# Performance work log

Measured on AMD Instinct MI355X. Metric: run time of the kernel, lower is better.

## Reference

```python
import jax, jax.numpy as jnp
import numpy as np


def setup_inputs() -> dict:
    key = jax.random.key(0)
    k1, k2 = jax.random.split(key)
    B, La, Lb, D = 32, 512, 512, 768
    a_bar = jax.random.normal(k1, (B, La, D), dtype=jnp.float32)
    b_bar = jax.random.normal(k2, (B, Lb, D), dtype=jnp.float32)
    return {"a_bar": a_bar, "b_bar": b_bar}


def reference(a_bar, b_bar):
    # e: [B, La, Lb] cross-attention scores
    e = jnp.einsum('bad,bcd->bac', a_bar, b_bar)
    # attend over b positions (softmax dim=2) -> aligned representation of a
    a_tilde = jnp.einsum('bac,bcd->bad', jax.nn.softmax(e, axis=2), b_bar)
    # attend over a positions (softmax dim=1), transpose, bmm with a_bar
    b_tilde = jnp.einsum('bac,bad->bcd', jax.nn.softmax(e, axis=1), a_bar)
    m_a = jnp.concatenate([a_bar, a_tilde, a_bar - a_tilde, a_bar * a_tilde], axis=-1)
    m_b = jnp.concatenate([b_bar, b_tilde, b_bar - b_tilde, b_bar * b_tilde], axis=-1)
    return (m_a, m_b)
```

## Files before the change

kernel.cpp:

```cpp
#include <hip/hip_runtime.h>
#include <hip/hip_bf16.h>
#include <math.h>

#define NB 32
#define LA 512
#define LB 512
#define DD 768

typedef __bf16 bf16x4 __attribute__((ext_vector_type(4)));
typedef __bf16 bf16x8 __attribute__((ext_vector_type(8)));
typedef float f32x4 __attribute__((ext_vector_type(4)));

#define LSTR 40

__device__ __forceinline__ void gload_lds16(const void* g, void* l) {
  __builtin_amdgcn_global_load_lds(
      (const __attribute__((address_space(1))) unsigned int*)g,
      (__attribute__((address_space(3))) unsigned int*)l, 16, 0, 0);
}

__global__ __launch_bounds__(256) void convert_kernel(
    const float* __restrict__ A, const float* __restrict__ B,
    __bf16* __restrict__ Ah, __bf16* __restrict__ Al,
    __bf16* __restrict__ Bh, __bf16* __restrict__ Bl,
    __bf16* __restrict__ AhT, __bf16* __restrict__ BhT) {
  const int zb = blockIdx.z;
  const int b = zb & (NB - 1);
  const bool isB = zb >= NB;
  const float* src = (isB ? B : A) + (size_t)b * 512 * DD;
  __bf16* H = (isB ? Bh : Ah) + (size_t)b * 512 * DD;
  __bf16* L = (isB ? Bl : Al) + (size_t)b * 512 * DD;
  __bf16* T = (isB ? BhT : AhT) + (size_t)b * DD * 512;
  const int d0 = blockIdx.x * 64, i0 = blockIdx.y * 64;
  __shared__ __bf16 Tt[64][72];
  const int t = threadIdx.x;
  const int c4 = t & 15, r = t >> 4;
#pragma unroll
  for (int p = 0; p < 4; ++p) {
    const int i = i0 + r + p * 16;
    const float4 v = *(const float4*)(src + (size_t)i * DD + d0 + c4 * 4);
    float vv[4] = {v.x, v.y, v.z, v.w};
    bf16x4 h, l;
#pragma unroll
    for (int q = 0; q < 4; ++q) {
      h[q] = (__bf16)vv[q];
      l[q] = (__bf16)(vv[q] - (float)h[q]);
    }
    *(bf16x4*)(H + (size_t)i * DD + d0 + c4 * 4) = h;
    *(bf16x4*)(L + (size_t)i * DD + d0 + c4 * 4) = l;
#pragma unroll
    for (int q = 0; q < 4; ++q) Tt[c4 * 4 + q][r + p * 16] = h[q];
  }
  __syncthreads();
  const int cc = t & 7, rr = t >> 3;
#pragma unroll
  for (int p = 0; p < 2; ++p) {
    const int d = d0 + rr + p * 32;
    *(bf16x8*)(T + (size_t)d * 512 + i0 + cc * 8) =
        *(bf16x8*)&Tt[rr + p * 32][cc * 8];
  }
}

__global__ __launch_bounds__(256) void gemm_e_mfma(
    const __bf16* __restrict__ Ah, const __bf16* __restrict__ Al,
    const __bf16* __restrict__ Bh, const __bf16* __restrict__ Bl,
    float* __restrict__ E) {
  __shared__ __bf16 S[2][4][128][32];

  const int id = blockIdx.x;
  const int wg = (id & 7) * 64 + (id >> 3);
  const int b = wg >> 4, tl = wg & 15;
  const int i0 = (tl & 3) * 128, j0 = (tl >> 2) * 128;

  const __bf16* AhB = Ah + (size_t)b * LA * DD;
  const __bf16* AlB = Al + (size_t)b * LA * DD;
  const __bf16* BhB = Bh + (size_t)b * LB * DD;
  const __bf16* BlB = Bl + (size_t)b * LB * DD;
  float* Eb = E + (size_t)b * LA * LB;

  const int t = threadIdx.x;
  const int lane = t & 63, wave = t >> 6;
  const int wm = (wave >> 1) * 64, wn = (wave & 1) * 64;
  const int quad = lane >> 4, l16 = lane & 15;
  const int lrow = lane >> 2, lcol = (lane & 3) * 8;

  auto stage = [&](int buf, int k0) {
#pragma unroll
    for (int n = 0; n < 2; ++n) {
      const int c = n * 4 + wave;
      const int row = c * 16 + lrow;
      const size_t gA = (size_t)(i0 + row) * DD + k0 + lcol;
      const size_t gB = (size_t)(j0 + row) * DD + k0 + lcol;
      char* base = (char*)&S[buf][0][0][0];
      gload_lds16(AhB + gA, base + c * 1024);
      gload_lds16(AlB + gA, base + 8192 + c * 1024);
      gload_lds16(BhB + gB, base + 16384 + c * 1024);
      gload_lds16(BlB + gB, base + 24576 + c * 1024);
    }
  };

  f32x4 acc[4][4] = {};

  stage(0, 0);
  __syncthreads();
  int cur = 0;
  for (int k0 = 0; k0 < DD; k0 += 32) {
    if (k0 + 32 < DD) stage(cur ^ 1, k0 + 32);

    bf16x8 fah[4], fal[4], fbh[4], fbl[4];
#pragma unroll
    for (int f = 0; f < 4; ++f) {
      fah[f] = *(bf16x8*)&S[cur][0][wm + f * 16 + l16][quad * 8];
      fal[f] = *(bf16x8*)&S[cur][1][wm + f * 16 + l16][quad * 8];
      fbh[f] = *(bf16x8*)&S[cur][2][wn + f * 16 + l16][quad * 8];
      fbl[f] = *(bf16x8*)&S[cur][3][wn + f * 16 + l16][quad * 8];
    }
#pragma unroll
    for (int fm = 0; fm < 4; ++fm)
#pragma unroll
      for (int fn = 0; fn < 4; ++fn) {
        acc[fm][fn] = __builtin_amdgcn_mfma_f32_16x16x32_bf16(fah[fm], fbh[fn], acc[fm][fn], 0, 0, 0);
        acc[fm][fn] = __builtin_amdgcn_mfma_f32_16x16x32_bf16(fah[fm], fbl[fn], acc[fm][fn], 0, 0, 0);
        acc[fm][fn] = __builtin_amdgcn_mfma_f32_16x16x32_bf16(fal[fm], fbh[fn], acc[fm][fn], 0, 0, 0);
      }
    __syncthreads();
    cur ^= 1;
  }

#pragma unroll
  for (int fm = 0; fm < 4; ++fm)
#pragma unroll
    for (int r = 0; r < 4; ++r) {
      const int i = i0 + wm + fm * 16 + quad * 4 + r;
#pragma unroll
      for (int fn = 0; fn < 4; ++fn)
        Eb[(size_t)i * LB + j0 + wn + fn * 16 + l16] = acc[fm][fn][r];
    }
}

__global__ __launch_bounds__(256) void row_stats_kernel(
    const float* __restrict__ E, float* __restrict__ rmax,
    float* __restrict__ rsum) {
  const int wave = threadIdx.x >> 6;
  const int lane = threadIdx.x & 63;
  const int row = blockIdx.x * 4 + wave;
  const float* Er = E + (size_t)row * LB;
  float vals[8];
  float m = -INFINITY;
#pragma unroll
  for (int c = 0; c < 8; ++c) {
    vals[c] = Er[lane + c * 64];
    m = fmaxf(m, vals[c]);
  }
#pragma unroll
  for (int off = 32; off > 0; off >>= 1) m = fmaxf(m, __shfl_xor(m, off));
  float s = 0.f;
#pragma unroll
  for (int c = 0; c < 8; ++c) s += __expf(vals[c] - m);
#pragma unroll
  for (int off = 32; off > 0; off >>= 1) s += __shfl_xor(s, off);
  if (lane == 0) { rmax[row] = m; rsum[row] = s; }
}

__global__ __launch_bounds__(256) void col_partial(
    const float* __restrict__ E, float* __restrict__ pcm,
    float* __restrict__ pcs) {
  const int c = blockIdx.x * 256 + threadIdx.x;
  const int b = c >> 9, j = c & (LB - 1);
  const int i0 = blockIdx.y * 64;
  const float* Ep = E + ((size_t)b * LA + i0) * LB + j;
  float m = -INFINITY, s = 0.f;
#pragma unroll 4
  for (int i = 0; i < 64; ++i) {
    const float v = Ep[(size_t)i * LB];
    const float mn = fmaxf(m, v);
    s = s * __expf(m - mn) + __expf(v - mn);
    m = mn;
  }
  pcm[blockIdx.y * (NB * LB) + c] = m;
  pcs[blockIdx.y * (NB * LB) + c] = s;
}

__global__ __launch_bounds__(256) void col_combine(
    const float* __restrict__ pcm, const float* __restrict__ pcs,
    float* __restrict__ cmax, float* __restrict__ csum) {
  const int c = blockIdx.x * 256 + threadIdx.x;
  float m = -INFINITY, s = 0.f;
#pragma unroll
  for (int p = 0; p < 8; ++p) {
    const float mp = pcm[p * (NB * LB) + c];
    const float sp = pcs[p * (NB * LB) + c];
    const float mn = fmaxf(m, mp);
    s = s * __expf(m - mn) + sp * __expf(mp - mn);
    m = mn;
  }
  cmax[c] = m;
  csum[c] = s;
}

__global__ __launch_bounds__(256) void gemm_at_mfma(
    const float* __restrict__ E, const __bf16* __restrict__ BhT,
    const float* __restrict__ A, const float* __restrict__ rmax,
    const float* __restrict__ rsum, float* __restrict__ Ma) {
  __shared__ __bf16 Ps[2][128][LSTR];
  __shared__ __bf16 Bs[2][128][32];
  __shared__ float rm_s[128], rs_s[128];

  const int id = blockIdx.x;
  const int wg = (id & 7) * 96 + (id >> 3);
  const int b = wg / 24, r24 = wg % 24;
  const int i0 = (r24 / 6) * 128, d0 = (r24 % 6) * 128;

  const float* Eb = E + (size_t)b * LA * LB;
  const __bf16* Tb = BhT + (size_t)b * DD * LB;
  const float* Ab = A + (size_t)b * LA * DD;

  const int t = threadIdx.x;
  const int lane = t & 63, wave = t >> 6;
  const int wm = (wave >> 1) * 64, wn = (wave & 1) * 64;
  const int quad = lane >> 4, l16 = lane & 15;
  const int sr = t >> 3, sc = t & 7;
  const int lrow = lane >> 2, lcol = (lane & 3) * 8;

  if (t < 128) {
    rm_s[t] = rmax[b * LA + i0 + t];
    rs_s[t] = 1.f / rsum[b * LA + i0 + t];
  }
  __syncthreads();

  auto loadE = [&](int k0, float4* ev) {
#pragma unroll
    for (int p = 0; p < 4; ++p)
      ev[p] = *(const float4*)(Eb + (size_t)(i0 + sr + p * 32) * LB + k0 + sc * 4);
  };
  auto stageB = [&](int buf, int k0) {
#pragma unroll
    for (int n = 0; n < 2; ++n) {
      const int c = n * 4 + wave;
      gload_lds16(Tb + (size_t)(d0 + c * 16 + lrow) * LB + k0 + lcol,
                  (char*)&Bs[buf][0][0] + c * 1024);
    }
  };
  auto writeP = [&](int buf, const float4* ev) {
#pragma unroll
    for (int p = 0; p < 4; ++p) {
      const int m = sr + p * 32;
      const float rmv = rm_s[m], rsv = rs_s[m];
      float v[4] = {ev[p].x, ev[p].y, ev[p].z, ev[p].w};
      bf16x4 pb;
#pragma unroll
      for (int q = 0; q < 4; ++q) pb[q] = (__bf16)(__expf(v[q] - rmv) * rsv);
      *(bf16x4*)&Ps[buf][m][sc * 4] = pb;
    }
  };

  f32x4 acc[4][4] = {};

  float4 ev[4];
  loadE(0, ev);
  stageB(0, 0);
  writeP(0, ev);
  __syncthreads();
  int cur = 0;
  for (int k0 = 0; k0 < LB; k0 += 32) {
    const bool nxt = (k0 + 32 < LB);
    float4 evn[4];
    if (nxt) { loadE(k0 + 32, evn); stageB(cur ^ 1, k0 + 32); }

    bf16x8 fa[4], fb[4];
#pragma unroll
    for (int f = 0; f < 4; ++f) {
      fa[f] = *(bf16x8*)&Ps[cur][wm + f * 16 + l16][quad * 8];
      fb[f] = *(bf16x8*)&Bs[cur][wn + f * 16 + l16][quad * 8];
    }
#pragma unroll
    for (int fm = 0; fm < 4; ++fm)
#pragma unroll
      for (int fn = 0; fn < 4; ++fn)
        acc[fm][fn] = __builtin_amdgcn_mfma_f32_16x16x32_bf16(fa[fm], fb[fn], acc[fm][fn], 0, 0, 0);

    if (nxt) writeP(cur ^ 1, evn);
    __syncthreads();
    cur ^= 1;
  }

#pragma unroll
  for (int fm = 0; fm < 4; ++fm)
#pragma unroll
    for (int r = 0; r < 4; ++r) {
      const int i = i0 + wm + fm * 16 + quad * 4 + r;
      float* base = Ma + ((size_t)b * LA + i) * (4 * DD);
#pragma unroll
      for (int fn = 0; fn < 4; ++fn) {
        const int d = d0 + wn + fn * 16 + l16;
        const float av = Ab[(size_t)i * DD + d];
        const float at = acc[fm][fn][r];
        base[d] = av;
        base[DD + d] = at;
        base[2 * DD + d] = av - at;
        base[3 * DD + d] = av * at;
      }
    }
}

__global__ __launch_bounds__(256) void gemm_bt_mfma(
    const float* __restrict__ E, const __bf16* __restrict__ AhT,
    const float* __restrict__ Bm, const float* __restrict__ cmax,
    const float* __restrict__ csum, float* __restrict__ Mb) {
  __shared__ __bf16 Ps[2][128][LSTR];
  __shared__ __bf16 As[2][128][32];
  __shared__ float cm_s[128], cs_s[128];

  const int id = blockIdx.x;
  const int wg = (id & 7) * 96 + (id >> 3);
  const int b = wg / 24, r24 = wg % 24;
  const int j0 = (r24 / 6) * 128, d0 = (r24 % 6) * 128;

  const float* Eb = E + (size_t)b * LA * LB;
  const __bf16* Tb = AhT + (size_t)b * DD * LA;
  const float* Bb = Bm + (size_t)b * LB * DD;

  const int t = threadIdx.x;
  const int lane = t & 63, wave = t >> 6;
  const int wm = (wave >> 1) * 64, wn = (wave & 1) * 64;
  const int quad = lane >> 4, l16 = lane & 15;
  const int ir = t >> 3, ic = t & 7;
  const int lrow = lane >> 2, lcol = (lane & 3) * 8;

  if (t < 128) {
    cm_s[t] = cmax[b * LB + j0 + t];
    cs_s[t] = 1.f / csum[b * LB + j0 + t];
  }
  __syncthreads();

  auto loadE = [&](int k0, float4* ev) {
#pragma unroll
    for (int p = 0; p < 4; ++p)
      ev[p] = *(const float4*)(Eb + (size_t)(k0 + ir) * LB + j0 + p * 32 + ic * 4);
  };
  auto stageA = [&](int buf, int k0) {
#pragma unroll
    for (int n = 0; n < 2; ++n) {
      const int c = n * 4 + wave;
      gload_lds16(Tb + (size_t)(d0 + c * 16 + lrow) * LA + k0 + lcol,
                  (char*)&As[buf][0][0] + c * 1024);
    }
  };
  auto writeP = [&](int buf, const float4* ev) {
#pragma unroll
    for (int p = 0; p < 4; ++p) {
      const float4 cm4 = *(const float4*)&cm_s[p * 32 + ic * 4];
      const float4 cs4 = *(const float4*)&cs_s[p * 32 + ic * 4];
      float v[4] = {ev[p].x, ev[p].y, ev[p].z, ev[p].w};
      float cmv[4] = {cm4.x, cm4.y, cm4.z, cm4.w};
      float csv[4] = {cs4.x, cs4.y, cs4.z, cs4.w};
#pragma unroll
      for (int q = 0; q < 4; ++q)
        Ps[buf][p * 32 + ic * 4 + q][ir] = (__bf16)(__expf(v[q] - cmv[q]) * csv[q]);
    }
  };

  f32x4 acc[4][4] = {};

  float4 ev[4];
  loadE(0, ev);
  stageA(0, 0);
  writeP(0, ev);
  __syncthreads();
  int cur = 0;
  for (int k0 = 0; k0 < LA; k0 += 32) {
    const bool nxt = (k0 + 32 < LA);
    float4 evn[4];
    if (nxt) { loadE(k0 + 32, evn); stageA(cur ^ 1, k0 + 32); }

    bf16x8 fa[4], fb[4];
#pragma unroll
    for (int f = 0; f < 4; ++f) {
      fa[f] = *(bf16x8*)&Ps[cur][wm + f * 16 + l16][quad * 8];
      fb[f] = *(bf16x8*)&As[cur][wn + f * 16 + l16][quad * 8];
    }
#pragma unroll
    for (int fm = 0; fm < 4; ++fm)
#pragma unroll
      for (int fn = 0; fn < 4; ++fn)
        acc[fm][fn] = __builtin_amdgcn_mfma_f32_16x16x32_bf16(fa[fm], fb[fn], acc[fm][fn], 0, 0, 0);

    if (nxt) writeP(cur ^ 1, evn);
    __syncthreads();
    cur ^= 1;
  }

#pragma unroll
  for (int fm = 0; fm < 4; ++fm)
#pragma unroll
    for (int r = 0; r < 4; ++r) {
      const int j = j0 + wm + fm * 16 + quad * 4 + r;
      float* base = Mb + ((size_t)b * LB + j) * (4 * DD);
#pragma unroll
      for (int fn = 0; fn < 4; ++fn) {
        const int d = d0 + wn + fn * 16 + l16;
        const float bvv = Bb[(size_t)j * DD + d];
        const float bt = acc[fm][fn][r];
        base[d] = bvv;
        base[DD + d] = bt;
        base[2 * DD + d] = bvv - bt;
        base[3 * DD + d] = bvv * bt;
      }
    }
}

extern "C" void kernel_launch(void* const* d_in, const int* in_sizes, int n_in,
                              void* d_out, int out_size, void* d_ws,
                              size_t ws_size, hipStream_t stream) {
  const float* a = (const float*)d_in[0];
  const float* bb = (const float*)d_in[1];
  float* out = (float*)d_out;
  float* Ma = out;
  float* Mb = out + (size_t)NB * LA * 4 * DD;

  char* p = (char*)d_ws;
  float* E = (float*)p;      p += (size_t)NB * LA * LB * 4;
  float* rmax = (float*)p;   p += (size_t)NB * LA * 4;
  float* rsum = (float*)p;   p += (size_t)NB * LA * 4;
  float* cmax = (float*)p;   p += (size_t)NB * LB * 4;
  float* csum = (float*)p;   p += (size_t)NB * LB * 4;
  float* pcm = (float*)p;    p += (size_t)8 * NB * LB * 4;
  float* pcs = (float*)p;    p += (size_t)8 * NB * LB * 4;
  __bf16* Ah = (__bf16*)p;   p += (size_t)NB * LA * DD * 2;
  __bf16* Al = (__bf16*)p;   p += (size_t)NB * LA * DD * 2;
  __bf16* Bh = (__bf16*)p;   p += (size_t)NB * LB * DD * 2;
  __bf16* Bl = (__bf16*)p;   p += (size_t)NB * LB * DD * 2;
  __bf16* AhT = (__bf16*)p;  p += (size_t)NB * DD * LA * 2;
  __bf16* BhT = (__bf16*)p;  p += (size_t)NB * DD * LB * 2;

  convert_kernel<<<dim3(DD / 64, 512 / 64, 2 * NB), 256, 0, stream>>>(
      a, bb, Ah, Al, Bh, Bl, AhT, BhT);
  gemm_e_mfma<<<dim3(512), 256, 0, stream>>>(Ah, Al, Bh, Bl, E);
  row_stats_kernel<<<dim3(NB * LA / 4), 256, 0, stream>>>(E, rmax, rsum);
  col_partial<<<dim3(NB * LB / 256, 8), 256, 0, stream>>>(E, pcm, pcs);
  col_combine<<<dim3(NB * LB / 256), 256, 0, stream>>>(pcm, pcs, cmax, csum);
  gemm_at_mfma<<<dim3(768), 256, 0, stream>>>(E, BhT, a, rmax, rsum, Ma);
  gemm_bt_mfma<<<dim3(768), 256, 0, stream>>>(E, AhT, bb, cmax, csum, Mb);
}
```

Before: 684.2 us.

## Precompute softmax probabilities in a separate pass and share one GEMM kernel

Adds a pconvert kernel that reads E once and writes both the row-softmax probabilities and the transposed column-softmax probabilities as bf16. The two attention GEMMs become one generic kernel that streams both operands into LDS with async global-to-LDS loads. Previously each GEMM block recomputed exp on E tiles that were re-read once per d-tile, six times in total. The change removes that redundant E traffic and exp work, and it drops the strided LDS transpose write. In exchange it adds an extra kernel launch plus bf16 write and read traffic for the two probability matrices.

```diff
diff --git a/kernel.cpp b/kernel.cpp
--- a/kernel.cpp
+++ b/kernel.cpp
@@ -10,8 +10,6 @@
 typedef __bf16 bf16x4 __attribute__((ext_vector_type(4)));
 typedef __bf16 bf16x8 __attribute__((ext_vector_type(8)));
 typedef float f32x4 __attribute__((ext_vector_type(4)));
-
-#define LSTR 40
 
 __device__ __forceinline__ void gload_lds16(const void* g, void* l) {
   __builtin_amdgcn_global_load_lds(
@@ -198,88 +196,99 @@
   csum[c] = s;
 }
 
-__global__ __launch_bounds__(256) void gemm_at_mfma(
-    const float* __restrict__ E, const __bf16* __restrict__ BhT,
-    const float* __restrict__ A, const float* __restrict__ rmax,
-    const float* __restrict__ rsum, float* __restrict__ Ma) {
-  __shared__ __bf16 Ps[2][128][LSTR];
-  __shared__ __bf16 Bs[2][128][32];
-  __shared__ float rm_s[128], rs_s[128];
+__global__ __launch_bounds__(256) void pconvert(
+    const float* __restrict__ E, const float* __restrict__ rmax,
+    const float* __restrict__ rsum, const float* __restrict__ cmax,
+    const float* __restrict__ csum, __bf16* __restrict__ Pa,
+    __bf16* __restrict__ PbT) {
+  const int b = blockIdx.z;
+  const int i0 = blockIdx.x * 128, j0 = blockIdx.y * 128;
+  const float* Eb = E + (size_t)b * LA * LB;
+  __shared__ __bf16 T[128][136];
+
+  const int t = threadIdx.x;
+  const int jr = t & 31, ir = t >> 5;
+  const float4 cm4 = *(const float4*)&cmax[b * LB + j0 + jr * 4];
+  const float4 cs4 = *(const float4*)&csum[b * LB + j0 + jr * 4];
+  const float cmv[4] = {cm4.x, cm4.y, cm4.z, cm4.w};
+  const float csv[4] = {1.f / cs4.x, 1.f / cs4.y, 1.f / cs4.z, 1.f / cs4.w};
+
+#pragma unroll
+  for (int p = 0; p < 16; ++p) {
+    const int i = i0 + ir + p * 8;
+    const float rm = rmax[b * LA + i];
+    const float rs = 1.f / rsum[b * LA + i];
+    const float4 v4 = *(const float4*)(Eb + (size_t)i * LB + j0 + jr * 4);
+    const float v[4] = {v4.x, v4.y, v4.z, v4.w};
+    bf16x4 pa;
+#pragma unroll
+    for (int q = 0; q < 4; ++q) {
+      pa[q] = (__bf16)(__expf(v[q] - rm) * rs);
+      T[jr * 4 + q][ir + p * 8] = (__bf16)(__expf(v[q] - cmv[q]) * csv[q]);
+    }
+    *(bf16x4*)(Pa + ((size_t)b * LA + i) * LB + j0 + jr * 4) = pa;
+  }
+  __syncthreads();
+  const int jl = t >> 4, ch = t & 15;
+#pragma unroll
+  for (int p = 0; p < 8; ++p) {
+    const int j = jl + p * 16;
+    *(bf16x8*)(PbT + ((size_t)b * LB + j0 + j) * LA + i0 + ch * 8) =
+        *(bf16x8*)&T[j][ch * 8];
+  }
+}
+
+__global__ __launch_bounds__(256) void gemm_pd(
+    const __bf16* __restrict__ P, const __bf16* __restrict__ T,
+    const float* __restrict__ S, float* __restrict__ Mout) {
+  __shared__ __bf16 Ls[2][2][128][32];
 
   const int id = blockIdx.x;
   const int wg = (id & 7) * 96 + (id >> 3);
   const int b = wg / 24, r24 = wg % 24;
-  const int i0 = (r24 / 6) * 128, d0 = (r24 % 6) * 128;
-
-  const float* Eb = E + (size_t)b * LA * LB;
-  const __bf16* Tb = BhT + (size_t)b * DD * LB;
-  const float* Ab = A + (size_t)b * LA * DD;
+  const int m0 = (r24 / 6) * 128, d0 = (r24 % 6) * 128;
+
+  const __bf16* Pb = P + (size_t)b * 512 * 512;
+  const __bf16* Tb = T + (size_t)b * DD * 512;
+  const float* Sb = S + (size_t)b * 512 * DD;
 
   const int t = threadIdx.x;
   const int lane = t & 63, wave = t >> 6;
   const int wm = (wave >> 1) * 64, wn = (wave & 1) * 64;
   const int quad = lane >> 4, l16 = lane & 15;
-  const int sr = t >> 3, sc = t & 7;
   const int lrow = lane >> 2, lcol = (lane & 3) * 8;
 
-  if (t < 128) {
-    rm_s[t] = rmax[b * LA + i0 + t];
-    rs_s[t] = 1.f / rsum[b * LA + i0 + t];
-  }
-  __syncthreads();
-
-  auto loadE = [&](int k0, float4* ev) {
-#pragma unroll
-    for (int p = 0; p < 4; ++p)
-      ev[p] = *(const float4*)(Eb + (size_t)(i0 + sr + p * 32) * LB + k0 + sc * 4);
-  };
-  auto stageB = [&](int buf, int k0) {
+  auto stage = [&](int buf, int k0) {
 #pragma unroll
     for (int n = 0; n < 2; ++n) {
       const int c = n * 4 + wave;
-      gload_lds16(Tb + (size_t)(d0 + c * 16 + lrow) * LB + k0 + lcol,
-                  (char*)&Bs[buf][0][0] + c * 1024);
+      const int row = c * 16 + lrow;
+      char* base = (char*)&Ls[buf][0][0][0];
+      gload_lds16(Pb + (size_t)(m0 + row) * 512 + k0 + lcol, base + c * 1024);
+      gload_lds16(Tb + (size_t)(d0 + row) * 512 + k0 + lcol,
+                  base + 8192 + c * 1024);
     }
   };
-  auto writeP = [&](int buf, const float4* ev) {
-#pragma unroll
-    for (int p = 0; p < 4; ++p) {
-      const int m = sr + p * 32;
-      const float rmv = rm_s[m], rsv = rs_s[m];
-      float v[4] = {ev[p].x, ev[p].y, ev[p].z, ev[p].w};
-      bf16x4 pb;
-#pragma unroll
-      for (int q = 0; q < 4; ++q) pb[q] = (__bf16)(__expf(v[q] - rmv) * rsv);
-      *(bf16x4*)&Ps[buf][m][sc * 4] = pb;
-    }
-  };
 
   f32x4 acc[4][4] = {};
 
-  float4 ev[4];
-  loadE(0, ev);
-  stageB(0, 0);
-  writeP(0, ev);
+  stage(0, 0);
   __syncthreads();
   int cur = 0;
-  for (int k0 = 0; k0 < LB; k0 += 32) {
-    const bool nxt = (k0 + 32 < LB);
-    float4 evn[4];
-    if (nxt) { loadE(k0 + 32, evn); stageB(cur ^ 1, k0 + 32); }
+  for (int k0 = 0; k0 < 512; k0 += 32) {
+    if (k0 + 32 < 512) stage(cur ^ 1, k0 + 32);
 
     bf16x8 fa[4], fb[4];
 #pragma unroll
     for (int f = 0; f < 4; ++f) {
-      fa[f] = *(bf16x8*)&Ps[cur][wm + f * 16 + l16][quad * 8];
-      fb[f] = *(bf16x8*)&Bs[cur][wn + f * 16 + l16][quad * 8];
+      fa[f] = *(bf16x8*)&Ls[cur][0][wm + f * 16 + l16][quad * 8];
+      fb[f] = *(bf16x8*)&Ls[cur][1][wn + f * 16 + l16][quad * 8];
     }
 #pragma unroll
     for (int fm = 0; fm < 4; ++fm)
 #pragma unroll
       for (int fn = 0; fn < 4; ++fn)
         acc[fm][fn] = __builtin_amdgcn_mfma_f32_16x16x32_bf16(fa[fm], fb[fn], acc[fm][fn], 0, 0, 0);
-
-    if (nxt) writeP(cur ^ 1, evn);
     __syncthreads();
     cur ^= 1;
   }
@@ -288,123 +297,18 @@
   for (int fm = 0; fm < 4; ++fm)
 #pragma unroll
     for (int r = 0; r < 4; ++r) {
-      const int i = i0 + wm + fm * 16 + quad * 4 + r;
-      float* base = Ma + ((size_t)b * LA + i) * (4 * DD);
+      const int m = m0 + wm + fm * 16 + quad * 4 + r;
+      float* base = Mout + ((size_t)b * 512 + m) * (4 * DD);
+      const float* srow = Sb + (size_t)m * DD;
 #pragma unroll
       for (int fn = 0; fn < 4; ++fn) {
         const int d = d0 + wn + fn * 16 + l16;
-        const float av = Ab[(size_t)i * DD + d];
-        const float at = acc[fm][fn][r];
-        base[d] = av;
-        base[DD + d] = at;
-        base[2 * DD + d] = av - at;
-        base[3 * DD + d] = av * at;
-      }
-    }
-}
-
-__global__ __launch_bounds__(256) void gemm_bt_mfma(
-    const float* __restrict__ E, const __bf16* __restrict__ AhT,
-    const float* __restrict__ Bm, const float* __restrict__ cmax,
-    const float* __restrict__ csum, float* __restrict__ Mb) {
-  __shared__ __bf16 Ps[2][128][LSTR];
-  __shared__ __bf16 As[2][128][32];
-  __shared__ float cm_s[128], cs_s[128];
-
-  const int id = blockIdx.x;
-  const int wg = (id & 7) * 96 + (id >> 3);
-  const int b = wg / 24, r24 = wg % 24;
-  const int j0 = (r24 / 6) * 128, d0 = (r24 % 6) * 128;
-
-  const float* Eb = E + (size_t)b * LA * LB;
-  const __bf16* Tb = AhT + (size_t)b * DD * LA;
-  const float* Bb = Bm + (size_t)b * LB * DD;
-
-  const int t = threadIdx.x;
-  const int lane = t & 63, wave = t >> 6;
-  const int wm = (wave >> 1) * 64, wn = (wave & 1) * 64;
-  const int quad = lane >> 4, l16 = lane & 15;
-  const int ir = t >> 3, ic = t & 7;
-  const int lrow = lane >> 2, lcol = (lane & 3) * 8;
-
-  if (t < 128) {
-    cm_s[t] = cmax[b * LB + j0 + t];
-    cs_s[t] = 1.f / csum[b * LB + j0 + t];
-  }
-  __syncthreads();
-
-  auto loadE = [&](int k0, float4* ev) {
-#pragma unroll
-    for (int p = 0; p < 4; ++p)
-      ev[p] = *(const float4*)(Eb + (size_t)(k0 + ir) * LB + j0 + p * 32 + ic * 4);
-  };
-  auto stageA = [&](int buf, int k0) {
-#pragma unroll
-    for (int n = 0; n < 2; ++n) {
-      const int c = n * 4 + wave;
-      gload_lds16(Tb + (size_t)(d0 + c * 16 + lrow) * LA + k0 + lcol,
-                  (char*)&As[buf][0][0] + c * 1024);
-    }
-  };
-  auto writeP = [&](int buf, const float4* ev) {
-#pragma unroll
-    for (int p = 0; p < 4; ++p) {
-      const float4 cm4 = *(const float4*)&cm_s[p * 32 + ic * 4];
-      const float4 cs4 = *(const float4*)&cs_s[p * 32 + ic * 4];
-      float v[4] = {ev[p].x, ev[p].y, ev[p].z, ev[p].w};
-      float cmv[4] = {cm4.x, cm4.y, cm4.z, cm4.w};
-      float csv[4] = {cs4.x, cs4.y, cs4.z, cs4.w};
-#pragma unroll
-      for (int q = 0; q < 4; ++q)
-        Ps[buf][p * 32 + ic * 4 + q][ir] = (__bf16)(__expf(v[q] - cmv[q]) * csv[q]);
-    }
-  };
-
-  f32x4 acc[4][4] = {};
-
-  float4 ev[4];
-  loadE(0, ev);
-  stageA(0, 0);
-  writeP(0, ev);
-  __syncthreads();
-  int cur = 0;
-  for (int k0 = 0; k0 < LA; k0 += 32) {
-    const bool nxt = (k0 + 32 < LA);
-    float4 evn[4];
-    if (nxt) { loadE(k0 + 32, evn); stageA(cur ^ 1, k0 + 32); }
-
-    bf16x8 fa[4], fb[4];
-#pragma unroll
-    for (int f = 0; f < 4; ++f) {
-      fa[f] = *(bf16x8*)&Ps[cur][wm + f * 16 + l16][quad * 8];
-      fb[f] = *(bf16x8*)&As[cur][wn + f * 16 + l16][quad * 8];
-    }
-#pragma unroll
-    for (int fm = 0; fm < 4; ++fm)
-#pragma unroll
-      for (int fn = 0; fn < 4; ++fn)
-        acc[fm][fn] = __builtin_amdgcn_mfma_f32_16x16x32_bf16(fa[fm], fb[fn], acc[fm][fn], 0, 0, 0);
-
-    if (nxt) writeP(cur ^ 1, evn);
-    __syncthreads();
-    cur ^= 1;
-  }
-
-#pragma unroll
-  for (int fm = 0; fm < 4; ++fm)
-#pragma unroll
-    for (int r = 0; r < 4; ++r) {
-      const int j = j0 + wm + fm * 16 + quad * 4 + r;
-      float* base = Mb + ((size_t)b * LB + j) * (4 * DD);
-#pragma unroll
-      for (int fn = 0; fn < 4; ++fn) {
-        const int d = d0 + wn + fn * 16 + l16;
-        const float bvv = Bb[(size_t)j * DD + d];
-        const float bt = acc[fm][fn][r];
-        base[d] = bvv;
-        base[DD + d] = bt;
-        base[2 * DD + d] = bvv - bt;
-        base[3 * DD + d] = bvv * bt;
+        const float sv = srow[d];
+        const float tv = acc[fm][fn][r];
+        base[d] = sv;
+        base[DD + d] = tv;
+        base[2 * DD + d] = sv - tv;
+        base[3 * DD + d] = sv * tv;
       }
     }
 }
@@ -432,6 +336,8 @@
   __bf16* Bl = (__bf16*)p;   p += (size_t)NB * LB * DD * 2;
   __bf16* AhT = (__bf16*)p;  p += (size_t)NB * DD * LA * 2;
   __bf16* BhT = (__bf16*)p;  p += (size_t)NB * DD * LB * 2;
+  __bf16* Pa = (__bf16*)p;   p += (size_t)NB * LA * LB * 2;
+  __bf16* PbT = (__bf16*)p;  p += (size_t)NB * LB * LA * 2;
 
   convert_kernel<<<dim3(DD / 64, 512 / 64, 2 * NB), 256, 0, stream>>>(
       a, bb, Ah, Al, Bh, Bl, AhT, BhT);
@@ -439,6 +345,8 @@
   row_stats_kernel<<<dim3(NB * LA / 4), 256, 0, stream>>>(E, rmax, rsum);
   col_partial<<<dim3(NB * LB / 256, 8), 256, 0, stream>>>(E, pcm, pcs);
   col_combine<<<dim3(NB * LB / 256), 256, 0, stream>>>(pcm, pcs, cmax, csum);
-  gemm_at_mfma<<<dim3(768), 256, 0, stream>>>(E, BhT, a, rmax, rsum, Ma);
-  gemm_bt_mfma<<<dim3(768), 256, 0, stream>>>(E, AhT, bb, cmax, csum, Mb);
-}
+  pconvert<<<dim3(LA / 128, LB / 128, NB), 256, 0, stream>>>(E, rmax, rsum,
+                                                             cmax, csum, Pa, PbT);
+  gemm_pd<<<dim3(768), 256, 0, stream>>>(Pa, BhT, a, Ma);
+  gemm_pd<<<dim3(768), 256, 0, stream>>>(PbT, AhT, bb, Mb);
+}
```

After: 672.7 us. Within noise of the previous version (-1.7%).
